# Performance work log

Hardware: AMD Instinct MI355X
Metric: run time of the kernel (lower is better)

Reference implementation:

```python
import jax, jax.numpy as jnp
import numpy as np

B, N, CIN = 8, 4096, 64
S, K, C = 1024, 32, 128      # npoint, k, out_channels
J, DEPTH, H = 5, 2, 4
BETA, EPS = 0.05, 1e-5


def _fps(xyz, npoint):
    # farthest point sampling, deterministic start at index 0
    Bb, Nn = xyz.shape[0], xyz.shape[1]
    bidx = jnp.arange(Bb)

    def step(carry, _):
        dist, far = carry
        cen = xyz[bidx, far][:, None, :]              # [B,1,3]
        d = jnp.sum((xyz - cen) ** 2, -1)             # [B,N]
        dist = jnp.minimum(dist, d)
        nxt = jnp.argmax(dist, axis=1).astype(jnp.int32)
        return (dist, nxt), far

    init = (jnp.full((Bb, Nn), 1e10, xyz.dtype), jnp.zeros((Bb,), jnp.int32))
    _, idxs = jax.lax.scan(step, init, None, length=npoint)
    return idxs.T                                      # [B,npoint]


def _ln(x, g, b):
    mu = jnp.mean(x, -1, keepdims=True)
    v = jnp.mean((x - mu) ** 2, -1, keepdims=True)
    return (x - mu) * jax.lax.rsqrt(v + EPS) * g + b


def _forward(xyz, points, w1, g1, b1, w2, g2, b2, w3, g3, b3,
             ws, wb, alpha, wqkv, wo, ln1g, ln1b, ln2g, ln2b):
    gather = jax.vmap(lambda a, i: a[i])
    fps_idx = _fps(xyz, S)
    new_xyz = gather(xyz, fps_idx)                     # [B,S,3]
    # kNN: squared distances from centroids to all points
    d2 = (jnp.sum(new_xyz ** 2, -1)[:, :, None] + jnp.sum(xyz ** 2, -1)[:, None, :]
          - 2.0 * jnp.einsum('bsd,bnd->bsn', new_xyz, xyz))   # [B,S,N]
    idx = jax.lax.top_k(-d2, K)[1]                     # [B,S,K]
    flat = idx.reshape(B, S * K)
    gxyz = gather(xyz, flat).reshape(B, S, K, 3)
    gnorm = gxyz - new_xyz[:, :, None, :]              # relative coords
    gpts = gather(points, flat).reshape(B, S, K, CIN)
    h = jnp.concatenate([gnorm, gpts], -1)             # [B,S,K,67]
    # pointwise shared MLP (1x1 conv + BN(batch stats) + ReLU)
    for w, g, b in ((w1, g1, b1), (w2, g2, b2), (w3, g3, b3)):
        h = jnp.einsum('bskc,oc->bsko', h, w)
        m = jnp.mean(h, (0, 1, 2))
        v = jnp.var(h, (0, 1, 2))
        h = jax.nn.relu((h - m) * jax.lax.rsqrt(v + EPS) * g + b)
    P = B * S
    pf = h.reshape(P, K, C)
    px = gnorm.reshape(P, K, 3)
    # per-patch graph: Gaussian affinity, sigma = mean pairwise distance
    dd = jnp.sum((px[:, :, None] - px[:, None, :]) ** 2, -1)   # [P,K,K]
    sigma = jnp.mean(jnp.sqrt(dd + 1e-12), (1, 2))[:, None, None]
    A = jnp.exp(-dd / (2.0 * sigma ** 2 + 1e-12))
    dinv = jax.lax.rsqrt(jnp.sum(A, -1) + 1e-12)
    I = jnp.eye(K, dtype=pf.dtype)
    L = I - dinv[:, :, None] * A * dinv[:, None, :]
    # heat-kernel wavelets psi_j = exp(-s_j L), 4th-order Taylor
    psis = []
    for j in range(J):
        M = (-BETA * (2.0 ** j)) * L
        T = I + M
        acc = M
        for m in range(2, 5):
            acc = jnp.einsum('pkl,plm->pkm', acc, M) / m
            T = T + acc
        psis.append(T)
    hcur = pf
    for d in range(DEPTH):
        mix = jnp.zeros_like(hcur)
        for j in range(J):
            mix = mix + alpha[d, j] * jnp.einsum('pkl,plc,cd->pkd', psis[j], hcur, ws[d, j])
        hcur = _ln(hcur + jax.nn.relu(mix + wb[d]), ln1g[d], ln1b[d])
        qkv = (hcur @ wqkv[d]).reshape(P, K, 3, H, C // H)
        q, k_, v = qkv[:, :, 0], qkv[:, :, 1], qkv[:, :, 2]      # [P,K,H,dh]
        att = jax.nn.softmax(jnp.einsum('pkhd,plhd->phkl', q, k_) / np.sqrt(C // H).astype(np.float32), axis=-1)
        o = jnp.einsum('phkl,plhd->pkhd', att, v).reshape(P, K, C) @ wo[d]
        hcur = _ln(hcur + o, ln2g[d], ln2b[d])
    out = jnp.max(hcur.reshape(B, S, K, C), axis=2)    # max-pool over k
    return new_xyz, out


def setup_inputs() -> dict:
    key = jax.random.key(0)
    ks = jax.random.split(key, 10)
    nrm = lambda k, shp, sc: jax.random.normal(k, shp, jnp.float32) * sc
    cin = CIN + 3
    return {
        'xyz': jax.random.normal(ks[0], (B, N, 3), jnp.float32),
        'points': jax.random.normal(ks[1], (B, N, CIN), jnp.float32),
        'w1': nrm(ks[2], (64, cin), cin ** -0.5),
        'g1': jnp.ones((64,)), 'b1': jnp.zeros((64,)),
        'w2': nrm(ks[3], (64, 64), 64 ** -0.5),
        'g2': jnp.ones((64,)), 'b2': jnp.zeros((64,)),
        'w3': nrm(ks[4], (C, 64), 64 ** -0.5),
        'g3': jnp.ones((C,)), 'b3': jnp.zeros((C,)),
        'ws': nrm(ks[5], (DEPTH, J, C, C), C ** -0.5),
        'wb': jnp.zeros((DEPTH, C)),
        'alpha': jnp.ones((DEPTH, J)) / J,
        'wqkv': nrm(ks[6], (DEPTH, C, 3 * C), C ** -0.5),
        'wo': nrm(ks[7], (DEPTH, C, C), C ** -0.5),
        'ln1g': jnp.ones((DEPTH, C)), 'ln1b': jnp.zeros((DEPTH, C)),
        'ln2g': jnp.ones((DEPTH, C)), 'ln2b': jnp.zeros((DEPTH, C)),
    }


def reference(xyz, points, w1, g1, b1, w2, g2, b2, w3, g3, b3,
              ws, wb, alpha, wqkv, wo, ln1g, ln1b, ln2g, ln2b):
    return _forward(xyz, points, w1, g1, b1, w2, g2, b2, w3, g3, b3,
                    ws, wb, alpha, wqkv, wo, ln1g, ln1b, ln2g, ln2b)
```

## Files before the change

kernel.cpp:

```cpp
#include <hip/hip_runtime.h>
#include <math.h>

#define NB 8
#define NP 4096
#define NCIN 64
#define NS 1024
#define NK 32
#define NC 128
#define NJ 5
#define NDEPTH 2
#define NH 4
#define NPTS (NB*NS)
#define NM (NPTS*NK)
#define EPSF 1e-5f

typedef float f32x4 __attribute__((ext_vector_type(4)));
typedef short bf16x8 __attribute__((ext_vector_type(8)));
typedef unsigned short ushort_t;
typedef unsigned long long u64;

#define MFMA(a,b,c) __builtin_amdgcn_mfma_f32_16x16x32_bf16(a,b,c,0,0,0)

__device__ __forceinline__ ushort_t f2b(float f) {
  unsigned int u = __float_as_uint(f);
  u = (u + 0x7fffu + ((u >> 16) & 1u)) >> 16;
  return (ushort_t)u;
}
__device__ __forceinline__ float b2f(ushort_t h) {
  unsigned int u = ((unsigned int)h) << 16;
  return __uint_as_float(u);
}

template<int CTRL>
__device__ __forceinline__ float dpp_f(float v) {
  return __int_as_float(__builtin_amdgcn_update_dpp(0, __float_as_int(v), CTRL, 0xf, 0xf, true));
}
__device__ __forceinline__ float dpp_sum16(float v) {
  v += dpp_f<0xB1>(v); v += dpp_f<0x4E>(v);
  v += dpp_f<0x141>(v); v += dpp_f<0x140>(v);
  return v;
}
__device__ __forceinline__ float dpp_max16(float v) {
  v = fmaxf(v, dpp_f<0xB1>(v)); v = fmaxf(v, dpp_f<0x4E>(v));
  v = fmaxf(v, dpp_f<0x141>(v)); v = fmaxf(v, dpp_f<0x140>(v));
  return v;
}

#define DPPMAX(CTRL) { \
  unsigned lo2 = (unsigned)__builtin_amdgcn_update_dpp(0, (int)(unsigned)best, CTRL, 0xf, 0xf, true); \
  unsigned hi2 = (unsigned)__builtin_amdgcn_update_dpp(0, (int)(unsigned)(best >> 32), CTRL, 0xf, 0xf, true); \
  u64 o = ((u64)hi2 << 32) | lo2; \
  if (o > best) best = o; }

__global__ __launch_bounds__(256) void k_fps(const float* __restrict__ xyz,
                                             float* __restrict__ newxyz) {
  const int b = blockIdx.x;
  const int t = threadIdx.x;
  const int lane = t & 63;
  const int w = t >> 6;
  __shared__ float Xl[NP*3];
  __shared__ float cenL[NS*3];
  __shared__ u64 slotP[2][4];
  __shared__ __align__(16) float slotC[2][4][4];
  const float* X = xyz + (size_t)b * NP * 3;
  for (int i = t; i < NP*3; i += 256) Xl[i] = X[i];
  __syncthreads();
  float px[16], py[16], pz[16], dist[16];
  unsigned inv[16];
#pragma unroll
  for (int i = 0; i < 16; ++i) {
    int n = t + 256*i;
    px[i] = Xl[3*n]; py[i] = Xl[3*n+1]; pz[i] = Xl[3*n+2];
    dist[i] = 1e10f;
    inv[i] = ~(unsigned)n;
  }
  float cx = Xl[0], cy = Xl[1], cz = Xl[2];
  for (int s = 0; s < NS; ++s) {
    if (t == 0) { cenL[3*s] = cx; cenL[3*s+1] = cy; cenL[3*s+2] = cz; }
    u64 pk[16];
#pragma unroll
    for (int i = 0; i < 16; ++i) {
      float dx = px[i]-cx, dy = py[i]-cy, dz = pz[i]-cz;
      float d = fmaf(dx,dx, fmaf(dy,dy, dz*dz));
      float nd = fminf(dist[i], d);
      dist[i] = nd;
      pk[i] = ((u64)__float_as_uint(nd) << 32) | inv[i];
    }
#pragma unroll
    for (int st = 1; st < 16; st <<= 1)
#pragma unroll
      for (int i = 0; i < 16; i += 2*st)
        pk[i] = pk[i+st] > pk[i] ? pk[i+st] : pk[i];
    u64 best = pk[0];
    DPPMAX(0x111)
    DPPMAX(0x112)
    DPPMAX(0x114)
    DPPMAX(0x118)
    DPPMAX(0x142)
    DPPMAX(0x143)
    if (lane == 63) {
      slotP[s&1][w] = best;
      int bi3 = 3 * (int)(~(unsigned)best);
      slotC[s&1][w][0] = Xl[bi3];
      slotC[s&1][w][1] = Xl[bi3+1];
      slotC[s&1][w][2] = Xl[bi3+2];
    }
    __syncthreads();
    const int par = s & 1;
    u64 s0 = slotP[par][0], s1 = slotP[par][1], s2 = slotP[par][2], s3 = slotP[par][3];
    f32x4 c0v = *(const f32x4*)&slotC[par][0][0];
    f32x4 c1v = *(const f32x4*)&slotC[par][1][0];
    f32x4 c2v = *(const f32x4*)&slotC[par][2][0];
    f32x4 c3v = *(const f32x4*)&slotC[par][3][0];
    u64 m = s0; f32x4 cw = c0v;
    if (s1 > m) { m = s1; cw = c1v; }
    if (s2 > m) { m = s2; cw = c2v; }
    if (s3 > m) { m = s3; cw = c3v; }
    cx = cw[0]; cy = cw[1]; cz = cw[2];
  }
  __syncthreads();
  float* o = newxyz + (size_t)b * NS * 3;
  for (int i = t; i < NS*3; i += 256) o[i] = cenL[i];
}

__global__ __launch_bounds__(64) void k_knn(const float* __restrict__ xyz,
                                            const float* __restrict__ newxyz,
                                            int* __restrict__ knn_idx,
                                            float* __restrict__ gnorm) {
  const int p = blockIdx.x;
  const int b = p >> 10;
  const int lane = threadIdx.x;
  const float* X = xyz + (size_t)b * NP * 3;
  __shared__ float d2[NP];
  float cx = newxyz[3*p], cy = newxyz[3*p+1], cz = newxyz[3*p+2];
  float sc = cx*cx + cy*cy + cz*cz;
#pragma unroll 4
  for (int i = 0; i < NP/64; ++i) {
    int n = lane + 64*i;
    float x = X[3*n], y = X[3*n+1], z = X[3*n+2];
    float sx = x*x + y*y + z*z;
    float dot = cx*x + cy*y + cz*z;
    d2[n] = sc + sx - 2.0f*dot;
  }
  for (int it = 0; it < NK; ++it) {
    float bv = 3.0e38f; int bi = 0x7fffffff;
#pragma unroll 8
    for (int i = 0; i < NP/64; ++i) {
      int n = lane + 64*i;
      float v = d2[n];
      if (v < bv) { bv = v; bi = n; }
    }
#pragma unroll
    for (int off = 32; off; off >>= 1) {
      float ov = __shfl_xor(bv, off);
      int   oi = __shfl_xor(bi, off);
      if (ov < bv || (ov == bv && oi < bi)) { bv = ov; bi = oi; }
    }
    if (lane == 0) {
      d2[bi] = 3.3e38f;
      knn_idx[p*NK + it] = bi;
      float* g = gnorm + ((size_t)p*NK + it)*3;
      g[0] = X[3*bi]   - cx;
      g[1] = X[3*bi+1] - cy;
      g[2] = X[3*bi+2] - cz;
    }
  }
}

__global__ __launch_bounds__(256) void k_layer1(const float* __restrict__ points,
                                                const int* __restrict__ knn_idx,
                                                const float* __restrict__ gnorm,
                                                const float* __restrict__ w1,
                                                float* __restrict__ y,
                                                float* __restrict__ stats) {
  const int r0 = blockIdx.x * 64;
  const int t = threadIdx.x;
  __shared__ float Xs[64][69];
  __shared__ float Ws[64][69];
  __shared__ int nid[64];
  __shared__ float ps[4][64], pss[4][64];
  if (t < 64) nid[t] = knn_idx[r0 + t];
  __syncthreads();
  for (int idx = t; idx < 64*67; idx += 256) {
    int r = idx / 67, c = idx % 67;
    int row = r0 + r;
    float v;
    if (c < 3) v = gnorm[(size_t)row*3 + c];
    else {
      int bb = row >> 15;
      int n = nid[r];
      v = points[((size_t)bb*NP + n)*NCIN + (c-3)];
    }
    Xs[r][c] = v;
  }
  for (int idx = t; idx < 64*67; idx += 256) {
    int o = idx / 67, c = idx % 67;
    Ws[o][c] = w1[idx];
  }
  __syncthreads();
  const int col = t & 63;
  const int rb  = t >> 6;
  float s1 = 0.f, s2 = 0.f;
  for (int i = 0; i < 16; ++i) {
    int r = rb + 4*i;
    float acc = 0.f;
#pragma unroll
    for (int c = 0; c < 67; ++c) acc += Xs[r][c] * Ws[col][c];
    y[(size_t)(r0 + r)*64 + col] = acc;
    s1 += acc; s2 += acc*acc;
  }
  ps[rb][col] = s1; pss[rb][col] = s2;
  __syncthreads();
  if (t < 64) {
    float a = ps[0][t]+ps[1][t]+ps[2][t]+ps[3][t];
    float q = pss[0][t]+pss[1][t]+pss[2][t]+pss[3][t];
    atomicAdd(&stats[t], a);
    atomicAdd(&stats[64 + t], q);
  }
}

template <int COUT>
__global__ __launch_bounds__(256) void k_layerM(const float* __restrict__ xin,
                                                const float* __restrict__ aff,
                                                const ushort_t* __restrict__ wp,
                                                float* __restrict__ y,
                                                float* __restrict__ stats) {
  const int r0 = blockIdx.x * 64;
  const int t = threadIdx.x;
  const int lane = t & 63;
  const int w = t >> 6;
  const int lo16 = lane & 15;
  const int hi4 = lane >> 4;
  constexpr int NTN = COUT >> 4;
  __shared__ __align__(16) ushort_t XbS[64*72];
  __shared__ float sa[64], sb[64];
  __shared__ float ps[4][COUT], pss[4][COUT];
  if (t < 64) { sa[t] = aff[t]; sb[t] = aff[64 + t]; }
  __syncthreads();
#pragma unroll
  for (int i = 0; i < 16; ++i) {
    int idx = t + 256*i;
    int r = idx >> 6, c = idx & 63;
    float v = xin[(size_t)r0*64 + idx];
    XbS[r*72 + c] = f2b(fmaxf(sa[c]*v + sb[c], 0.0f));
  }
  __syncthreads();
  const int arow = (w*16 + lo16)*72;
  float s1[NTN], s2[NTN];
#pragma unroll
  for (int tn = 0; tn < NTN; ++tn) {
    f32x4 acc = {0.f,0.f,0.f,0.f};
#pragma unroll
    for (int tk = 0; tk < 2; ++tk) {
      bf16x8 a = *(const bf16x8*)(XbS + arow + tk*32 + hi4*8);
      bf16x8 b = *(const bf16x8*)(wp + ((tk*NTN + tn) << 9) + (lane << 3));
      acc = MFMA(a, b, acc);
    }
    int col = tn*16 + lo16;
    int rbase = r0 + w*16 + hi4*4;
    float a1 = 0.f, a2 = 0.f;
#pragma unroll
    for (int r = 0; r < 4; ++r) {
      y[(size_t)(rbase + r)*COUT + col] = acc[r];
      a1 += acc[r]; a2 += acc[r]*acc[r];
    }
    a1 += __shfl_xor(a1, 16); a1 += __shfl_xor(a1, 32);
    a2 += __shfl_xor(a2, 16); a2 += __shfl_xor(a2, 32);
    s1[tn] = a1; s2[tn] = a2;
  }
  if (hi4 == 0) {
#pragma unroll
    for (int tn = 0; tn < NTN; ++tn) {
      ps[w][tn*16 + lo16]  = s1[tn];
      pss[w][tn*16 + lo16] = s2[tn];
    }
  }
  __syncthreads();
  if (t < COUT) {
    atomicAdd(&stats[t],        ps[0][t]+ps[1][t]+ps[2][t]+ps[3][t]);
    atomicAdd(&stats[COUT + t], pss[0][t]+pss[1][t]+pss[2][t]+pss[3][t]);
  }
}

__global__ void k_finalize(const float* __restrict__ stats, const float* __restrict__ g,
                           const float* __restrict__ b, float* __restrict__ aff, int cout) {
  int t = threadIdx.x;
  if (t < cout) {
    const float inv = 1.0f / (float)NM;
    float m = stats[t] * inv;
    float var = stats[cout + t] * inv - m*m;
    float a = g[t] * rsqrtf(var + EPSF);
    aff[t] = a;
    aff[cout + t] = b[t] - m * a;
  }
}

__global__ __launch_bounds__(256) void k_pack(const float* __restrict__ ws,
                                              const float* __restrict__ wqkv,
                                              const float* __restrict__ wo,
                                              const float* __restrict__ w2,
                                              const float* __restrict__ w3,
                                              ushort_t* __restrict__ wpk) {
  int gid = blockIdx.x*256 + threadIdx.x;
  if (gid < 294912) {
    const float* src; int N_; int rem;
    if (gid < 163840)      { int mat = gid >> 14; rem = gid & 16383; src = ws  + (size_t)mat*16384; N_ = 128; }
    else if (gid < 262144) { int g2 = gid - 163840; int d = g2/49152; rem = g2 - d*49152; src = wqkv + (size_t)d*49152; N_ = 384; }
    else                   { int g3 = gid - 262144; int d = g3 >> 14; rem = g3 & 16383;  src = wo  + (size_t)d*16384; N_ = 128; }
    int NTN = N_ >> 4;
    int tile = rem >> 9, r = rem & 511;
    int tk = tile / NTN, tn = tile % NTN;
    int lane2 = r >> 3, jj = r & 7;
    int k = tk*32 + (lane2 >> 4)*8 + jj;
    int n = tn*16 + (lane2 & 15);
    wpk[gid] = f2b(src[(size_t)k*N_ + n]);
  } else if (gid < 299008) {
    int rem = gid - 294912;
    int tile = rem >> 9, r = rem & 511;
    int tk = tile >> 2, tn = tile & 3;
    int lane2 = r >> 3, jj = r & 7;
    int k = tk*32 + (lane2 >> 4)*8 + jj;
    int n = tn*16 + (lane2 & 15);
    wpk[gid] = f2b(w2[n*64 + k]);
  } else if (gid < 307200) {
    int rem = gid - 299008;
    int tile = rem >> 9, r = rem & 511;
    int tk = tile >> 3, tn = tile & 7;
    int lane2 = r >> 3, jj = r & 7;
    int k = tk*32 + (lane2 >> 4)*8 + jj;
    int n = tn*16 + (lane2 & 15);
    wpk[gid] = f2b(w3[n*64 + k]);
  }
}

__global__ __launch_bounds__(256, 2) void k_group(
    const float* __restrict__ h3, const float* __restrict__ aff3,
    const float* __restrict__ gnorm,
    const ushort_t* __restrict__ wpk,
    const float* __restrict__ wb, const float* __restrict__ alpha,
    const float* __restrict__ ln1g, const float* __restrict__ ln1b,
    const float* __restrict__ ln2g, const float* __restrict__ ln2b,
    float* __restrict__ out) {
  const int p = blockIdx.x;
  const int t = threadIdx.x;
  const int lane = t & 63;
  const int w = t >> 6;
  const int lo16 = lane & 15;
  const int hi4 = lane >> 4;

  __shared__ __align__(16) ushort_t hbS[NK*NC];
  __shared__ __align__(16) ushort_t psisS[5*32*40];
  __shared__ __align__(16) unsigned char scratch[27648];

  float*    ddAF = (float*)scratch;
  float*    pxF  = (float*)(scratch + 4224);
  float*    dinvF= (float*)(scratch + 4608);
  float*    sigF = (float*)(scratch + 4736);
  ushort_t* LbS  = (ushort_t*)(scratch + 4768);
  ushort_t* PmS  = (ushort_t*)(scratch + 7328);
  ushort_t* qS   = (ushort_t*)scratch;
  ushort_t* kS2  = (ushort_t*)(scratch + 8704);
  ushort_t* vTS  = (ushort_t*)(scratch + 17408);
  float*    rowStat = (float*)(scratch + 20480);

  const int c0 = 32*w + lo16, c1 = c0 + 16;

  if (t < 96) pxF[t] = gnorm[(size_t)p*96 + t];
  const float* h3p = h3 + (size_t)p*4096;
#pragma unroll
  for (int i = 0; i < 16; ++i) {
    int idx = t + 256*i;
    int c = idx & 127, row = idx >> 7;
    float v = fmaxf(aff3[c]*h3p[idx] + aff3[128+c], 0.f);
    int ha = ((row << 8) + (c << 1)) ^ ((row & 7) << 4);
    hbS[ha >> 1] = f2b(v);
  }
  float hc[2][2][4];
  {
    float ga0 = aff3[c0], gb0 = aff3[128+c0];
    float ga1 = aff3[c1], gb1 = aff3[128+c1];
#pragma unroll
    for (int mi = 0; mi < 2; ++mi)
#pragma unroll
      for (int r = 0; r < 4; ++r) {
        int row = mi*16 + hi4*4 + r;
        hc[mi][0][r] = fmaxf(ga0*h3p[row*NC + c0] + gb0, 0.f);
        hc[mi][1][r] = fmaxf(ga1*h3p[row*NC + c1] + gb1, 0.f);
      }
  }
  __syncthreads();
  for (int i = t; i < 1024; i += 256) {
    int k = i >> 5, l = i & 31;
    float dx = pxF[k*3]  -pxF[l*3];
    float dy = pxF[k*3+1]-pxF[l*3+1];
    float dz = pxF[k*3+2]-pxF[l*3+2];
    ddAF[k*33+l] = dx*dx + dy*dy + dz*dz;
  }
  __syncthreads();
  float part = 0.f;
  for (int i = t; i < 1024; i += 256) part += sqrtf(ddAF[(i>>5)*33 + (i&31)] + 1e-12f);
#pragma unroll
  for (int off = 32; off; off >>= 1) part += __shfl_xor(part, off);
  if (lane == 0) sigF[w] = part;
  __syncthreads();
  if (t == 0) {
    float sg = (sigF[0]+sigF[1]+sigF[2]+sigF[3]) * (1.0f/1024.0f);
    sigF[4] = 2.0f*sg*sg + 1e-12f;
  }
  __syncthreads();
  const float denom = sigF[4];
  for (int i = t; i < 1024; i += 256) {
    int k = i >> 5, l = i & 31;
    ddAF[k*33+l] = expf(-ddAF[k*33+l] / denom);
  }
  __syncthreads();
  if (t < 32) {
    float s = 0.f;
    for (int l = 0; l < 32; ++l) s += ddAF[t*33 + l];
    dinvF[t] = rsqrtf(s + 1e-12f);
  }
  __syncthreads();
  for (int i = t; i < 1024; i += 256) {
    int k = i >> 5, l = i & 31;
    float v = -(dinvF[k] * ddAF[k*33+l] * dinvF[l]);
    if (k == l) v += 1.0f;
    LbS[k*40+l] = f2b(v);
  }
  __syncthreads();
  {
    int mi2 = w >> 1, ni2 = w & 1;
    int arow = (mi2*16 + lo16)*80 + (hi4 << 4);
    int brow = (ni2*16 + lo16)*80 + (hi4 << 4);
    bf16x8 bfr = *(const bf16x8*)((const char*)LbS + brow);
#pragma unroll
    for (int m = 2; m <= 4; ++m) {
      const ushort_t* Asrc = (m == 2) ? LbS : (PmS + (m-3)*1280);
      bf16x8 afr = *(const bf16x8*)((const char*)Asrc + arow);
      f32x4 z = {0.f,0.f,0.f,0.f};
      f32x4 pv = MFMA(afr, bfr, z);
      int rb2 = mi2*16 + hi4*4;
      int cl = ni2*16 + lo16;
#pragma unroll
      for (int r = 0; r < 4; ++r) PmS[(m-2)*1280 + (rb2+r)*40 + cl] = f2b(pv[r]);
      __syncthreads();
    }
  }
  for (int i = t; i < 1024; i += 256) {
    int k = i >> 5, l = i & 31;
    float lb = b2f(LbS[k*40+l]);
    float p2 = b2f(PmS[k*40+l]);
    float p3 = b2f(PmS[1280 + k*40+l]);
    float p4 = b2f(PmS[2560 + k*40+l]);
    float diag = (k == l) ? 1.0f : 0.0f;
#pragma unroll
    for (int j = 0; j < NJ; ++j) {
      float sj = -0.05f * (float)(1 << j);
      float cc2 = 0.5f*sj*sj;
      float cc3 = cc2*sj*(1.0f/3.0f);
      float cc4 = cc3*sj*0.25f;
      psisS[j*1280 + k*40 + l] = f2b(diag + sj*lb + cc2*p2 + cc3*p3 + cc4*p4);
    }
  }

  for (int d = 0; d < NDEPTH; ++d) {
    f32x4 m00 = {0.f,0.f,0.f,0.f}, m01 = m00, m10 = m00, m11 = m00;
    for (int jp = 0; jp < 3; ++jp) {
      const int njp = (jp == 2) ? 1 : 2;
      __syncthreads();
      for (int jj = 0; jj < njp; ++jj) {
        int j = 2*jp + jj;
        ushort_t* HjS = (ushort_t*)scratch + jj*5120;
        const ushort_t* Wp = wpk + (size_t)(d*NJ + j)*16384;
        const float alj = alpha[d*NJ + j];
#pragma unroll
        for (int tni = 0; tni < 2; ++tni) {
          int tn = 2*w + tni;
          f32x4 acc0 = {0.f,0.f,0.f,0.f}, acc1 = acc0;
#pragma unroll
          for (int tk = 0; tk < 4; ++tk) {
            bf16x8 bfr = *(const bf16x8*)(Wp + ((tk*8 + tn) << 9) + (lane << 3));
            int row0 = lo16;
            int ba0 = ((row0 << 8) + (tk << 6) + (hi4 << 4)) ^ ((row0 & 7) << 4);
            bf16x8 a0 = *(const bf16x8*)((const char*)hbS + ba0);
            acc0 = MFMA(a0, bfr, acc0);
            int row1 = 16 + lo16;
            int ba1 = ((row1 << 8) + (tk << 6) + (hi4 << 4)) ^ ((row1 & 7) << 4);
            bf16x8 a1 = *(const bf16x8*)((const char*)hbS + ba1);
            acc1 = MFMA(a1, bfr, acc1);
          }
          int c = tn*16 + lo16;
          int rbase = hi4*4;
#pragma unroll
          for (int r = 0; r < 4; ++r) {
            HjS[c*40 + rbase + r]      = f2b(alj * acc0[r]);
            HjS[c*40 + 16 + rbase + r] = f2b(alj * acc1[r]);
          }
        }
      }
      __syncthreads();
      for (int jj = 0; jj < njp; ++jj) {
        int j = 2*jp + jj;
        const char* psj = (const char*)(psisS + j*1280);
        const char* HjB = (const char*)scratch + jj*10240;
        int koff = hi4 << 4;
        bf16x8 pa0 = *(const bf16x8*)(psj + lo16*80 + koff);
        bf16x8 pa1 = *(const bf16x8*)(psj + (16 + lo16)*80 + koff);
        bf16x8 hb0 = *(const bf16x8*)(HjB + c0*80 + koff);
        bf16x8 hb1 = *(const bf16x8*)(HjB + c1*80 + koff);
        m00 = MFMA(pa0, hb0, m00);
        m01 = MFMA(pa0, hb1, m01);
        m10 = MFMA(pa1, hb0, m10);
        m11 = MFMA(pa1, hb1, m11);
      }
    }
    float u[2][2][4];
    {
      float wb0 = wb[d*NC + c0], wb1 = wb[d*NC + c1];
#pragma unroll
      for (int r = 0; r < 4; ++r) {
        u[0][0][r] = hc[0][0][r] + fmaxf(m00[r] + wb0, 0.f);
        u[0][1][r] = hc[0][1][r] + fmaxf(m01[r] + wb1, 0.f);
        u[1][0][r] = hc[1][0][r] + fmaxf(m10[r] + wb0, 0.f);
        u[1][1][r] = hc[1][1][r] + fmaxf(m11[r] + wb1, 0.f);
      }
#pragma unroll
      for (int mi = 0; mi < 2; ++mi)
#pragma unroll
        for (int r = 0; r < 4; ++r) {
          float s = u[mi][0][r] + u[mi][1][r];
          float q = u[mi][0][r]*u[mi][0][r] + u[mi][1][r]*u[mi][1][r];
          s = dpp_sum16(s);
          q = dpp_sum16(q);
          if (lo16 == 0) {
            int row = mi*16 + hi4*4 + r;
            rowStat[row*8 + w*2]     = s;
            rowStat[row*8 + w*2 + 1] = q;
          }
        }
    }
    __syncthreads();
    {
      float g0 = ln1g[d*NC + c0], b0 = ln1b[d*NC + c0];
      float g1 = ln1g[d*NC + c1], b1 = ln1b[d*NC + c1];
#pragma unroll
      for (int mi = 0; mi < 2; ++mi)
#pragma unroll
        for (int r = 0; r < 4; ++r) {
          int row = mi*16 + hi4*4 + r;
          f32x4 a = *(const f32x4*)(rowStat + row*8);
          f32x4 bq = *(const f32x4*)(rowStat + row*8 + 4);
          float mu = (a[0]+a[2]+bq[0]+bq[2]) * (1.0f/128.0f);
          float ex2 = (a[1]+a[3]+bq[1]+bq[3]) * (1.0f/128.0f);
          float rs = rsqrtf(ex2 - mu*mu + EPSF);
          float h0 = (u[mi][0][r] - mu)*rs*g0 + b0;
          float h1 = (u[mi][1][r] - mu)*rs*g1 + b1;
          hc[mi][0][r] = h0; hc[mi][1][r] = h1;
          int ha0 = ((row << 8) + (c0 << 1)) ^ ((row & 7) << 4);
          int ha1 = ((row << 8) + (c1 << 1)) ^ ((row & 7) << 4);
          hbS[ha0 >> 1] = f2b(h0);
          hbS[ha1 >> 1] = f2b(h1);
        }
    }
    __syncthreads();
    const ushort_t* Wq = wpk + 163840 + (size_t)d*49152;
#pragma unroll
    for (int ti = 0; ti < 12; ++ti) {
      int tile = w + 4*ti;
      int mi = (tile >= 24) ? 1 : 0;
      int tn = tile - 24*mi;
      int comp = tn >> 3;
      int cb = (tn & 7) * 16;
      f32x4 acc = {0.f,0.f,0.f,0.f};
#pragma unroll
      for (int tk = 0; tk < 4; ++tk) {
        bf16x8 bfr = *(const bf16x8*)(Wq + ((tk*24 + tn) << 9) + (lane << 3));
        int row = mi*16 + lo16;
        int ba = ((row << 8) + (tk << 6) + (hi4 << 4)) ^ ((row & 7) << 4);
        bf16x8 a = *(const bf16x8*)((const char*)hbS + ba);
        acc = MFMA(a, bfr, acc);
      }
      int cl = cb + lo16;
      int rb2 = mi*16 + hi4*4;
      if (comp == 0) {
#pragma unroll
        for (int r = 0; r < 4; ++r) qS[(rb2+r)*136 + cl] = f2b(acc[r]);
      } else if (comp == 1) {
#pragma unroll
        for (int r = 0; r < 4; ++r) kS2[(rb2+r)*136 + cl] = f2b(acc[r]);
      } else {
#pragma unroll
        for (int r = 0; r < 4; ++r) vTS[cl*40 + rb2 + r] = f2b(acc[r]);
      }
    }
    __syncthreads();
    float scr[2][2][4];
#pragma unroll
    for (int ti = 0; ti < 2; ++ti) {
      int pi = w + 4*ti;
      int h = pi >> 1, mi = pi & 1;
      int koff = h*64 + (hi4 << 4);
      bf16x8 qa = *(const bf16x8*)((const char*)qS + (mi*16 + lo16)*272 + koff);
#pragma unroll
      for (int ni = 0; ni < 2; ++ni) {
        bf16x8 kb = *(const bf16x8*)((const char*)kS2 + (ni*16 + lo16)*272 + koff);
        f32x4 z = {0.f,0.f,0.f,0.f};
        f32x4 sv = MFMA(qa, kb, z);
#pragma unroll
        for (int r = 0; r < 4; ++r) scr[ti][ni][r] = sv[r] * 0.17677669529663687f;
      }
    }
    __syncthreads();
#pragma unroll
    for (int ti = 0; ti < 2; ++ti) {
      int pi = w + 4*ti;
      int h = pi >> 1, mi = pi & 1;
#pragma unroll
      for (int r = 0; r < 4; ++r) {
        float s0 = scr[ti][0][r], s1 = scr[ti][1][r];
        float mx = dpp_max16(fmaxf(s0, s1));
        float e0 = expf(s0 - mx), e1 = expf(s1 - mx);
        float sum = dpp_sum16(e0 + e1);
        float iv = 1.0f / sum;
        int row = mi*16 + hi4*4 + r;
        qS[row*136 + h*32 + lo16]      = f2b(e0*iv);
        qS[row*136 + h*32 + 16 + lo16] = f2b(e1*iv);
      }
    }
    __syncthreads();
#pragma unroll
    for (int ti = 0; ti < 4; ++ti) {
      int tile = w + 4*ti;
      int h = tile >> 2, mi = (tile >> 1) & 1, ni = tile & 1;
      bf16x8 aa = *(const bf16x8*)((const char*)qS + (mi*16 + lo16)*272 + h*64 + (hi4 << 4));
      bf16x8 vb = *(const bf16x8*)((const char*)vTS + (h*32 + ni*16 + lo16)*80 + (hi4 << 4));
      f32x4 z = {0.f,0.f,0.f,0.f};
      f32x4 ov = MFMA(aa, vb, z);
      int col = h*32 + ni*16 + lo16;
      int rb2 = mi*16 + hi4*4;
#pragma unroll
      for (int r = 0; r < 4; ++r) {
        int row = rb2 + r;
        int ha = ((row << 8) + (col << 1)) ^ ((row & 7) << 4);
        hbS[ha >> 1] = f2b(ov[r]);
      }
    }
    __syncthreads();
    const ushort_t* Wop = wpk + 262144 + (size_t)d*16384;
#pragma unroll
    for (int tni = 0; tni < 2; ++tni) {
      int tn = 2*w + tni;
      f32x4 acc0 = {0.f,0.f,0.f,0.f}, acc1 = acc0;
#pragma unroll
      for (int tk = 0; tk < 4; ++tk) {
        bf16x8 bfr = *(const bf16x8*)(Wop + ((tk*8 + tn) << 9) + (lane << 3));
        int row0 = lo16;
        int ba0 = ((row0 << 8) + (tk << 6) + (hi4 << 4)) ^ ((row0 & 7) << 4);
        bf16x8 a0 = *(const bf16x8*)((const char*)hbS + ba0);
        acc0 = MFMA(a0, bfr, acc0);
        int row1 = 16 + lo16;
        int ba1 = ((row1 << 8) + (tk << 6) + (hi4 << 4)) ^ ((row1 & 7) << 4);
        bf16x8 a1 = *(const bf16x8*)((const char*)hbS + ba1);
        acc1 = MFMA(a1, bfr, acc1);
      }
#pragma unroll
      for (int r = 0; r < 4; ++r) {
        u[0][tni][r] = hc[0][tni][r] + acc0[r];
        u[1][tni][r] = hc[1][tni][r] + acc1[r];
      }
    }
#pragma unroll
    for (int mi = 0; mi < 2; ++mi)
#pragma unroll
      for (int r = 0; r < 4; ++r) {
        float s = u[mi][0][r] + u[mi][1][r];
        float q = u[mi][0][r]*u[mi][0][r] + u[mi][1][r]*u[mi][1][r];
        s = dpp_sum16(s);
        q = dpp_sum16(q);
        if (lo16 == 0) {
          int row = mi*16 + hi4*4 + r;
          rowStat[row*8 + w*2]     = s;
          rowStat[row*8 + w*2 + 1] = q;
        }
      }
    __syncthreads();
    {
      float g0 = ln2g[d*NC + c0], b0 = ln2b[d*NC + c0];
      float g1 = ln2g[d*NC + c1], b1 = ln2b[d*NC + c1];
#pragma unroll
      for (int mi = 0; mi < 2; ++mi)
#pragma unroll
        for (int r = 0; r < 4; ++r) {
          int row = mi*16 + hi4*4 + r;
          f32x4 a = *(const f32x4*)(rowStat + row*8);
          f32x4 bq = *(const f32x4*)(rowStat + row*8 + 4);
          float mu = (a[0]+a[2]+bq[0]+bq[2]) * (1.0f/128.0f);
          float ex2 = (a[1]+a[3]+bq[1]+bq[3]) * (1.0f/128.0f);
          float rs = rsqrtf(ex2 - mu*mu + EPSF);
          float h0 = (u[mi][0][r] - mu)*rs*g0 + b0;
          float h1 = (u[mi][1][r] - mu)*rs*g1 + b1;
          hc[mi][0][r] = h0; hc[mi][1][r] = h1;
          int ha0 = ((row << 8) + (c0 << 1)) ^ ((row & 7) << 4);
          int ha1 = ((row << 8) + (c1 << 1)) ^ ((row & 7) << 4);
          hbS[ha0 >> 1] = f2b(h0);
          hbS[ha1 >> 1] = f2b(h1);
        }
    }
  }
  {
    float v0 = hc[0][0][0], v1 = hc[0][1][0];
#pragma unroll
    for (int r = 1; r < 4; ++r) { v0 = fmaxf(v0, hc[0][0][r]); v1 = fmaxf(v1, hc[0][1][r]); }
#pragma unroll
    for (int r = 0; r < 4; ++r) { v0 = fmaxf(v0, hc[1][0][r]); v1 = fmaxf(v1, hc[1][1][r]); }
    v0 = fmaxf(v0, __shfl_xor(v0, 16)); v0 = fmaxf(v0, __shfl_xor(v0, 32));
    v1 = fmaxf(v1, __shfl_xor(v1, 16)); v1 = fmaxf(v1, __shfl_xor(v1, 32));
    if (hi4 == 0) {
      out[(size_t)p*NC + c0] = v0;
      out[(size_t)p*NC + c1] = v1;
    }
  }
}

extern "C" void kernel_launch(void* const* d_in, const int* in_sizes, int n_in,
                              void* d_out, int out_size, void* d_ws, size_t ws_size,
                              hipStream_t stream) {
  const float* xyz    = (const float*)d_in[0];
  const float* points = (const float*)d_in[1];
  const float* w1     = (const float*)d_in[2];
  const float* g1     = (const float*)d_in[3];
  const float* b1     = (const float*)d_in[4];
  const float* w2     = (const float*)d_in[5];
  const float* g2     = (const float*)d_in[6];
  const float* b2     = (const float*)d_in[7];
  const float* w3     = (const float*)d_in[8];
  const float* g3     = (const float*)d_in[9];
  const float* b3     = (const float*)d_in[10];
  const float* wsW    = (const float*)d_in[11];
  const float* wb     = (const float*)d_in[12];
  const float* alpha  = (const float*)d_in[13];
  const float* wqkv   = (const float*)d_in[14];
  const float* wo     = (const float*)d_in[15];
  const float* ln1g   = (const float*)d_in[16];
  const float* ln1b   = (const float*)d_in[17];
  const float* ln2g   = (const float*)d_in[18];
  const float* ln2b   = (const float*)d_in[19];
  float* outp = (float*)d_out;

  float* wsf   = (float*)d_ws;
  float* gnorm = wsf;
  float* stats = wsf + 786432;
  float* aff   = wsf + 787200;
  int*   knn   = (int*)(wsf + 787968);
  ushort_t* wpk = (ushort_t*)(wsf + 787968);
  float* h2    = wsf + 1050112;
  float* hX    = wsf + 17827328;

  hipMemsetAsync(stats, 0, 768*sizeof(float), stream);
  k_fps<<<NB, 256, 0, stream>>>(xyz, outp);
  k_knn<<<NPTS, 64, 0, stream>>>(xyz, outp, knn, gnorm);
  k_layer1<<<NM/64, 256, 0, stream>>>(points, knn, gnorm, w1, hX, stats);
  k_pack<<<307200/256, 256, 0, stream>>>(wsW, wqkv, wo, w2, w3, wpk);
  k_finalize<<<1, 128, 0, stream>>>(stats, g1, b1, aff, 64);
  k_layerM<64><<<NM/64, 256, 0, stream>>>(hX, aff, wpk + 294912, h2, stats + 256);
  k_finalize<<<1, 128, 0, stream>>>(stats + 256, g2, b2, aff + 256, 64);
  k_layerM<128><<<NM/64, 256, 0, stream>>>(h2, aff + 256, wpk + 299008, hX, stats + 512);
  k_finalize<<<1, 128, 0, stream>>>(stats + 512, g3, b3, aff + 512, 128);
  k_group<<<NPTS, 256, 0, stream>>>(hX, aff + 512, gnorm, wpk, wb, alpha,
                                    ln1g, ln1b, ln2g, ln2b, outp + (size_t)NB*NS*3);
}
```

Baseline: 1.807 ms.

## Use bf16 MFMA for first MLP layer and DPP reduction in kNN argmin

The first pointwise layer (67->64) moves from a scalar fp32 LDS dot-product to 16x16x32 bf16 MFMA, with w1 prepacked into MFMA tile order by a new small kernel and K padded to 96. The kNN selection loop replaces the 64-lane shuffle argmin with packed 64-bit key DPP min reductions followed by a broadcast from lane 63. This is meant to cut ALU and LDS cost in layer 1 and shuffle latency in the 32 serial kNN iterations. Layer 1 inputs now lose precision to bf16, which could perturb the batch statistics, and extra workspace is used for packed weights.

```diff
diff --git a/kernel.cpp b/kernel.cpp
--- a/kernel.cpp
+++ b/kernel.cpp
@@ -51,6 +51,12 @@
   unsigned hi2 = (unsigned)__builtin_amdgcn_update_dpp(0, (int)(unsigned)(best >> 32), CTRL, 0xf, 0xf, true); \
   u64 o = ((u64)hi2 << 32) | lo2; \
   if (o > best) best = o; }
+
+#define DPPMIN(CTRL) { \
+  unsigned lo2 = (unsigned)__builtin_amdgcn_update_dpp((int)(unsigned)best, (int)(unsigned)best, CTRL, 0xf, 0xf, false); \
+  unsigned hi2 = (unsigned)__builtin_amdgcn_update_dpp((int)(unsigned)(best >> 32), (int)(unsigned)(best >> 32), CTRL, 0xf, 0xf, false); \
+  u64 o = ((u64)hi2 << 32) | lo2; \
+  if (o < best) best = o; }
 
 __global__ __launch_bounds__(256) void k_fps(const float* __restrict__ xyz,
                                              float* __restrict__ newxyz) {
@@ -150,33 +156,53 @@
       float v = d2[n];
       if (v < bv) { bv = v; bi = n; }
     }
-#pragma unroll
-    for (int off = 32; off; off >>= 1) {
-      float ov = __shfl_xor(bv, off);
-      int   oi = __shfl_xor(bi, off);
-      if (ov < bv || (ov == bv && oi < bi)) { bv = ov; bi = oi; }
-    }
+    unsigned ub = __float_as_uint(bv);
+    ub ^= ((unsigned)((int)ub >> 31)) | 0x80000000u;
+    u64 best = ((u64)ub << 32) | (unsigned)bi;
+    DPPMIN(0x111)
+    DPPMIN(0x112)
+    DPPMIN(0x114)
+    DPPMIN(0x118)
+    DPPMIN(0x142)
+    DPPMIN(0x143)
+    u64 win = __shfl(best, 63);
     if (lane == 0) {
-      d2[bi] = 3.3e38f;
-      knn_idx[p*NK + it] = bi;
+      int wi = (int)(unsigned)win;
+      d2[wi] = 3.3e38f;
+      knn_idx[p*NK + it] = wi;
       float* g = gnorm + ((size_t)p*NK + it)*3;
-      g[0] = X[3*bi]   - cx;
-      g[1] = X[3*bi+1] - cy;
-      g[2] = X[3*bi+2] - cz;
-    }
-  }
-}
-
-__global__ __launch_bounds__(256) void k_layer1(const float* __restrict__ points,
-                                                const int* __restrict__ knn_idx,
-                                                const float* __restrict__ gnorm,
-                                                const float* __restrict__ w1,
-                                                float* __restrict__ y,
-                                                float* __restrict__ stats) {
+      g[0] = X[3*wi]   - cx;
+      g[1] = X[3*wi+1] - cy;
+      g[2] = X[3*wi+2] - cz;
+    }
+  }
+}
+
+__global__ __launch_bounds__(256) void k_pack1(const float* __restrict__ w1,
+                                               ushort_t* __restrict__ wp) {
+  int gid = blockIdx.x*256 + threadIdx.x;
+  int tile = gid >> 9, r = gid & 511;
+  int tk = tile >> 2, tn = tile & 3;
+  int lane2 = r >> 3, jj = r & 7;
+  int k = tk*32 + (lane2 >> 4)*8 + jj;
+  int n = tn*16 + (lane2 & 15);
+  float v = (k < 67) ? w1[n*67 + k] : 0.0f;
+  wp[gid] = f2b(v);
+}
+
+__global__ __launch_bounds__(256) void k_layer1M(const float* __restrict__ points,
+                                                 const int* __restrict__ knn_idx,
+                                                 const float* __restrict__ gnorm,
+                                                 const ushort_t* __restrict__ wp1,
+                                                 float* __restrict__ y,
+                                                 float* __restrict__ stats) {
   const int r0 = blockIdx.x * 64;
   const int t = threadIdx.x;
-  __shared__ float Xs[64][69];
-  __shared__ float Ws[64][69];
+  const int lane = t & 63;
+  const int w = t >> 6;
+  const int lo16 = lane & 15;
+  const int hi4 = lane >> 4;
+  __shared__ __align__(16) ushort_t XbS[64*104];
   __shared__ int nid[64];
   __shared__ float ps[4][64], pss[4][64];
   if (t < 64) nid[t] = knn_idx[r0 + t];
@@ -191,31 +217,47 @@
       int n = nid[r];
       v = points[((size_t)bb*NP + n)*NCIN + (c-3)];
     }
-    Xs[r][c] = v;
-  }
-  for (int idx = t; idx < 64*67; idx += 256) {
-    int o = idx / 67, c = idx % 67;
-    Ws[o][c] = w1[idx];
-  }
-  __syncthreads();
-  const int col = t & 63;
-  const int rb  = t >> 6;
-  float s1 = 0.f, s2 = 0.f;
-  for (int i = 0; i < 16; ++i) {
-    int r = rb + 4*i;
-    float acc = 0.f;
-#pragma unroll
-    for (int c = 0; c < 67; ++c) acc += Xs[r][c] * Ws[col][c];
-    y[(size_t)(r0 + r)*64 + col] = acc;
-    s1 += acc; s2 += acc*acc;
-  }
-  ps[rb][col] = s1; pss[rb][col] = s2;
+    XbS[r*104 + c] = f2b(v);
+  }
+  for (int idx = t; idx < 64*37; idx += 256) {
+    int r = idx / 37, c = idx % 37;
+    XbS[r*104 + 67 + c] = 0;
+  }
+  __syncthreads();
+  const int arow = (w*16 + lo16)*104;
+  float s1[4], s2[4];
+#pragma unroll
+  for (int tn = 0; tn < 4; ++tn) {
+    f32x4 acc = {0.f,0.f,0.f,0.f};
+#pragma unroll
+    for (int tk = 0; tk < 3; ++tk) {
+      bf16x8 a = *(const bf16x8*)(XbS + arow + tk*32 + hi4*8);
+      bf16x8 b = *(const bf16x8*)(wp1 + ((tk*4 + tn) << 9) + (lane << 3));
+      acc = MFMA(a, b, acc);
+    }
+    int col = tn*16 + lo16;
+    int rbase = r0 + w*16 + hi4*4;
+    float a1 = 0.f, a2 = 0.f;
+#pragma unroll
+    for (int r = 0; r < 4; ++r) {
+      y[(size_t)(rbase + r)*64 + col] = acc[r];
+      a1 += acc[r]; a2 += acc[r]*acc[r];
+    }
+    a1 += __shfl_xor(a1, 16); a1 += __shfl_xor(a1, 32);
+    a2 += __shfl_xor(a2, 16); a2 += __shfl_xor(a2, 32);
+    s1[tn] = a1; s2[tn] = a2;
+  }
+  if (hi4 == 0) {
+#pragma unroll
+    for (int tn = 0; tn < 4; ++tn) {
+      ps[w][tn*16 + lo16]  = s1[tn];
+      pss[w][tn*16 + lo16] = s2[tn];
+    }
+  }
   __syncthreads();
   if (t < 64) {
-    float a = ps[0][t]+ps[1][t]+ps[2][t]+ps[3][t];
-    float q = pss[0][t]+pss[1][t]+pss[2][t]+pss[3][t];
-    atomicAdd(&stats[t], a);
-    atomicAdd(&stats[64 + t], q);
+    atomicAdd(&stats[t],      ps[0][t]+ps[1][t]+ps[2][t]+ps[3][t]);
+    atomicAdd(&stats[64 + t], pss[0][t]+pss[1][t]+pss[2][t]+pss[3][t]);
   }
 }
 
@@ -754,11 +796,13 @@
   ushort_t* wpk = (ushort_t*)(wsf + 787968);
   float* h2    = wsf + 1050112;
   float* hX    = wsf + 17827328;
+  ushort_t* wp1 = (ushort_t*)(wsf + 17827328 + 16777216);
 
   hipMemsetAsync(stats, 0, 768*sizeof(float), stream);
   k_fps<<<NB, 256, 0, stream>>>(xyz, outp);
   k_knn<<<NPTS, 64, 0, stream>>>(xyz, outp, knn, gnorm);
-  k_layer1<<<NM/64, 256, 0, stream>>>(points, knn, gnorm, w1, hX, stats);
+  k_pack1<<<24, 256, 0, stream>>>(w1, wp1);
+  k_layer1M<<<NM/64, 256, 0, stream>>>(points, knn, gnorm, wp1, hX, stats);
   k_pack<<<307200/256, 256, 0, stream>>>(wsW, wqkv, wo, w2, w3, wpk);
   k_finalize<<<1, 128, 0, stream>>>(stats, g1, b1, aff, 64);
   k_layerM<64><<<NM/64, 256, 0, stream>>>(hX, aff, wpk + 294912, h2, stats + 256);
```

New measurement: 1.756 ms. -2.8%, faster.
